# Kernel optimization log

Measured on AMD Instinct MI355X. Metric: run time of the kernel, lower is better.

The kernel has to match this reference:

```python
import jax, jax.numpy as jnp
import numpy as np

E = 2048   # embed_dim
H = 16     # num query heads
D = E // H # head_dim = 128
B = 2
S = 2048


def setup_inputs() -> dict:
    key = jax.random.key(0)
    ks = jax.random.split(key, 12)
    sc = 0.02
    return {
        "input": jax.random.normal(ks[0], (B, S, E), jnp.float32),
        "kv": jax.random.normal(ks[1], (B, S, E), jnp.float32),
        "Wq": jax.random.normal(ks[2], (E, E), jnp.float32) * sc,
        "bq": jnp.zeros((E,), jnp.float32),
        "Wk": jax.random.normal(ks[3], (D, E), jnp.float32) * sc,
        "bk": jnp.zeros((D,), jnp.float32),
        "Wv": jax.random.normal(ks[4], (D, E), jnp.float32) * sc,
        "bv": jnp.zeros((D,), jnp.float32),
        "Wo": jax.random.normal(ks[5], (E, E), jnp.float32) * sc,
        "bo": jnp.zeros((E,), jnp.float32),
        "expanding_context": 0,
    }


def reference(input, kv, Wq, bq, Wk, bk, Wv, bv, Wo, bo, expanding_context):
    b, s, _ = input.shape
    # projections (torch Linear: x @ W.T + b)
    q = (input @ Wq.T + bq).reshape(b, s, H, D).transpose(0, 2, 1, 3)  # [B,H,S,D]
    k = kv @ Wk.T + bk  # [B,S,D] single KV head
    v = kv @ Wv.T + bv  # [B,S,D]
    # scores with single KV head broadcast across query heads
    scores = jnp.einsum('bhsd,btd->bhst', q, k) / jnp.sqrt(jnp.float32(D))
    causal = jnp.triu(jnp.ones((s, s), bool), k=1)  # True above diagonal
    scores = jnp.where(causal[None, None], jnp.float32(-jnp.inf), scores)
    attn = jax.nn.softmax(scores, axis=-1)
    out = jnp.einsum('bhst,btd->bhsd', attn, v)  # [B,H,S,D]
    out = out.transpose(0, 2, 1, 3).reshape(b, s, E)
    return out @ Wo.T + bo
```

## Files before the change

### kernel.cpp

```cpp
#include <hip/hip_runtime.h>

#define B_  2
#define S_  2048
#define E_  2048
#define H_  16
#define D_  128
#define BS_ (B_*S_)

typedef __bf16 bf16_t;
typedef __bf16 bf16x8 __attribute__((ext_vector_type(8)));
typedef __bf16 bf16x4 __attribute__((ext_vector_type(4)));
typedef float  f32x4  __attribute__((ext_vector_type(4)));
typedef float  f32x16 __attribute__((ext_vector_type(16)));

#define QSCALE 0.1275174131003543f

__device__ __forceinline__ void gld16(const bf16_t* g, bf16_t* l) {
    __builtin_amdgcn_global_load_lds(
        (const __attribute__((address_space(1))) void*)g,
        (__attribute__((address_space(3))) void*)l,
        16, 0, 0);
}

__global__ void cvt_all(const float* __restrict__ s0, const float* __restrict__ s1,
                        const float* __restrict__ s2, const float* __restrict__ s3,
                        const float* __restrict__ s4, const float* __restrict__ s5,
                        bf16_t* d0, bf16_t* d1, bf16_t* d2,
                        bf16_t* d3, bf16_t* d4, bf16_t* d5)
{
    long i = ((long)blockIdx.x * blockDim.x + threadIdx.x) * 4;
    const float* s; bf16_t* d;
    if      (i <  8388608) { s = s0; d = d0; }
    else if (i < 16777216) { s = s1; d = d1; i -=  8388608; }
    else if (i < 20971520) { s = s2; d = d2; i -= 16777216; }
    else if (i < 21233664) { s = s3; d = d3; i -= 20971520; }
    else if (i < 21495808) { s = s4; d = d4; i -= 21233664; }
    else                   { s = s5; d = d5; i -= 21495808; }
    float4 v = *(const float4*)(s + i);
    bf16x4 o;
    o[0] = (bf16_t)v.x; o[1] = (bf16_t)v.y; o[2] = (bf16_t)v.z; o[3] = (bf16_t)v.w;
    *(bf16x4*)(d + i) = o;
}

template<int EP>
__device__ __forceinline__ void gemm_tile64(
    const bf16_t* __restrict__ A, const bf16_t* __restrict__ W,
    const float* __restrict__ biasA, const float* __restrict__ biasB,
    float* __restrict__ Cf, bf16_t* __restrict__ Cb,
    int N, int K, float scale, int m0, int w_n0, int c_n0,
    bf16_t* As, bf16_t* Bs)
{
    const int tid  = threadIdx.x;
    const int wave = tid >> 6, lane = tid & 63;
    const int wm = wave >> 1, wn = wave & 1;
    const int lrow = lane & 15, quad = lane >> 4;
    const int r8 = lane >> 3, c8 = (lane & 7) << 3;

    f32x4 acc[4][2] = {};

    for (int k0 = 0; k0 < K; k0 += 64) {
        __syncthreads();
#pragma unroll
        for (int j = 0; j < 4; ++j) {
            int base = (wave * 4 + j) * 8;
            gld16(A + (size_t)(m0 + base + r8) * K + k0 + c8, &As[base * 64]);
        }
#pragma unroll
        for (int j = 0; j < 2; ++j) {
            int base = (wave * 2 + j) * 8;
            gld16(W + (size_t)(w_n0 + base + r8) * K + k0 + c8, &Bs[base * 64]);
        }
        __syncthreads();
#pragma unroll
        for (int ks = 0; ks < 2; ++ks) {
            bf16x8 af[4], bfr[2];
#pragma unroll
            for (int mt = 0; mt < 4; ++mt)
                af[mt] = *(const bf16x8*)&As[(wm * 64 + mt * 16 + lrow) * 64 + ks * 32 + quad * 8];
#pragma unroll
            for (int nt = 0; nt < 2; ++nt)
                bfr[nt] = *(const bf16x8*)&Bs[(wn * 32 + nt * 16 + lrow) * 64 + ks * 32 + quad * 8];
#pragma unroll
            for (int mt = 0; mt < 4; ++mt)
#pragma unroll
                for (int nt = 0; nt < 2; ++nt)
                    acc[mt][nt] = __builtin_amdgcn_mfma_f32_16x16x32_bf16(
                        af[mt], bfr[nt], acc[mt][nt], 0, 0, 0);
        }
    }

#pragma unroll
    for (int mt = 0; mt < 4; ++mt) {
#pragma unroll
        for (int nt = 0; nt < 2; ++nt) {
            int nn = wn * 32 + nt * 16 + lrow;
            int col = c_n0 + nn;
            float bvv = (EP == 1 && biasB && col >= 128) ? biasB[col - 128]
                                                         : biasA[col];
#pragma unroll
            for (int r = 0; r < 4; ++r) {
                int row = m0 + wm * 64 + mt * 16 + quad * 4 + r;
                float v = (acc[mt][nt][r] + bvv) * scale;
                if (EP == 0) Cf[(size_t)row * N + col] = v;
                else         Cb[(size_t)row * N + col] = (bf16_t)v;
            }
        }
    }
}

__global__ __launch_bounds__(256) void gemm_qkv(
    const bf16_t* __restrict__ xb, const bf16_t* __restrict__ kvb,
    const bf16_t* __restrict__ Wq, const bf16_t* __restrict__ Wkv,
    const float* __restrict__ bq, const float* __restrict__ bk,
    const float* __restrict__ bv,
    bf16_t* __restrict__ Qb, bf16_t* __restrict__ KVb)
{
    __shared__ __align__(16) bf16_t As[128 * 64];
    __shared__ __align__(16) bf16_t Bs[64 * 64];
    const int m0 = blockIdx.y * 128;
    if (blockIdx.x < 32) {
        int n0 = blockIdx.x * 64;
        gemm_tile64<1>(xb, Wq, bq, nullptr, nullptr, Qb, E_, E_, QSCALE,
                       m0, n0, n0, As, Bs);
    } else {
        int n0 = (blockIdx.x - 32) * 64;
        gemm_tile64<1>(kvb, Wkv, bk, bv, nullptr, KVb, 256, E_, 1.0f,
                       m0, n0, n0, As, Bs);
    }
}

__global__ __launch_bounds__(256) void gemm_o(
    const bf16_t* __restrict__ A, const bf16_t* __restrict__ W,
    const float* __restrict__ bias, float* __restrict__ Cf)
{
    __shared__ __align__(16) bf16_t As[128 * 64];
    __shared__ __align__(16) bf16_t Bs[64 * 64];
    int n0 = blockIdx.x * 64;
    gemm_tile64<0>(A, W, bias, nullptr, Cf, nullptr, E_, E_, 1.0f,
                   blockIdx.y * 128, n0, n0, As, Bs);
}

__global__ __launch_bounds__(256, 2) void mqa_attn(
    const bf16_t* __restrict__ Q, const bf16_t* __restrict__ KV,
    bf16_t* __restrict__ O)
{
    __shared__ __align__(16) bf16_t Kt[2][64][136];
    __shared__ __align__(16) bf16_t Vt[2][128][72];
    __shared__ float rsl[4][32];

    const int bx = blockIdx.x, h = blockIdx.y, b = blockIdx.z;
    const int qb = b ? bx : (15 - bx);
    const int tid = threadIdx.x, wave = tid >> 6, lane = tid & 63;
    const int ln = lane & 31, hi = lane >> 5;
    const int q0w = qb * 128 + wave * 32;

    const bf16_t* kvp = KV + (size_t)(b * S_) * 256;

    bf16x8 qf[8];
    {
        const bf16_t* qp = Q + ((size_t)(b * S_ + q0w + ln)) * E_ + h * D_ + hi * 8;
#pragma unroll
        for (int st = 0; st < 8; ++st) qf[st] = *(const bf16x8*)(qp + st * 16);
    }

    f32x16 oacc[4] = {};
    bf16x8 af[4] = {};
    float rs0 = 0.f, rs1 = 0.f, rs2 = 0.f, rs3 = 0.f;

    const int NT = 2 * qb + 2;
    const int Tw = (q0w + 31) >> 6;

    bf16x8 kreg[4], vreg[4];
    auto loadKV = [&](int kt) {
        const int k0 = kt * 64;
#pragma unroll
        for (int i = 0; i < 4; ++i) {
            int c = tid + 256 * i;
            kreg[i] = *(const bf16x8*)(kvp + (size_t)(k0 + (c >> 4)) * 256 + ((c & 15) << 3));
            int n = c & 63, d0 = (c >> 6) << 3;
            vreg[i] = *(const bf16x8*)(kvp + (size_t)(k0 + n) * 256 + 128 + d0);
        }
    };
    auto stageWrite = [&](int bb) {
#pragma unroll
        for (int i = 0; i < 4; ++i) {
            int c = tid + 256 * i;
            *(bf16x8*)&Kt[bb][c >> 4][(c & 15) << 3] = kreg[i];
            int n = c & 63, d0 = (c >> 6) << 3;
#pragma unroll
            for (int j = 0; j < 8; ++j) Vt[bb][d0 + j][n] = vreg[i][j];
        }
    };
    auto doPV = [&](int vb) {
        __builtin_amdgcn_s_setprio(1);
#pragma unroll
        for (int ks = 0; ks < 4; ++ks)
#pragma unroll
            for (int dt = 0; dt < 4; ++dt) {
                bf16x8 vf = *(const bf16x8*)&Vt[vb][dt * 32 + ln][ks * 16 + hi * 8];
                oacc[dt] = __builtin_amdgcn_mfma_f32_32x32x16_bf16(af[ks], vf, oacc[dt], 0, 0, 0);
            }
        __builtin_amdgcn_s_setprio(0);
    };

    loadKV(0);
    stageWrite(0);
    if (NT > 1) loadKV(1);

    for (int t = 0; t < NT; ++t) {
        const int cur = t & 1;
        if (t >= 1 && t - 1 <= Tw) doPV(cur ^ 1);
        __syncthreads();
        if (t + 1 < NT) stageWrite(cur ^ 1);
        if (t + 2 < NT) loadKV(t + 2);
        if (t <= Tw) {
            f32x16 sc[2] = {f32x16{}, f32x16{}};
            __builtin_amdgcn_s_setprio(1);
#pragma unroll
            for (int st = 0; st < 8; ++st) {
                bf16x8 qv = qf[st];
#pragma unroll
                for (int ct = 0; ct < 2; ++ct) {
                    bf16x8 kf = *(const bf16x8*)&Kt[cur][ct * 32 + ln][st * 16 + hi * 8];
                    sc[ct] = __builtin_amdgcn_mfma_f32_32x32x16_bf16(kf, qv, sc[ct], 0, 0, 0);
                }
            }
            __builtin_amdgcn_s_setprio(0);
            const int k_base = t * 64;
            const int qi = q0w + ln;
            if (k_base + 63 > q0w) {
#pragma unroll
                for (int ct = 0; ct < 2; ++ct)
#pragma unroll
                    for (int r = 0; r < 16; ++r) {
                        int kj = k_base + ct * 32 + (r & 3) + 8 * (r >> 2) + 4 * hi;
                        float s = (kj > qi) ? -1e30f : sc[ct][r];
                        float pv = exp2f(fminf(s, 110.f));
                        if ((r & 3) == 0) rs0 += pv;
                        else if ((r & 3) == 1) rs1 += pv;
                        else if ((r & 3) == 2) rs2 += pv;
                        else rs3 += pv;
                        sc[ct][r] = pv;
                    }
            } else {
#pragma unroll
                for (int ct = 0; ct < 2; ++ct)
#pragma unroll
                    for (int r = 0; r < 16; ++r) {
                        float pv = exp2f(fminf(sc[ct][r], 110.f));
                        if ((r & 3) == 0) rs0 += pv;
                        else if ((r & 3) == 1) rs1 += pv;
                        else if ((r & 3) == 2) rs2 += pv;
                        else rs3 += pv;
                        sc[ct][r] = pv;
                    }
            }
#pragma unroll
            for (int ks = 0; ks < 4; ++ks) {
                const int c = ks >> 1, b8 = (ks & 1) * 8;
                union { bf16_t h[2]; unsigned u; } pk0, pk1, pk2, pk3;
                pk0.h[0] = (bf16_t)sc[c][b8 + 0]; pk0.h[1] = (bf16_t)sc[c][b8 + 1];
                pk1.h[0] = (bf16_t)sc[c][b8 + 2]; pk1.h[1] = (bf16_t)sc[c][b8 + 3];
                pk2.h[0] = (bf16_t)sc[c][b8 + 4]; pk2.h[1] = (bf16_t)sc[c][b8 + 5];
                pk3.h[0] = (bf16_t)sc[c][b8 + 6]; pk3.h[1] = (bf16_t)sc[c][b8 + 7];
                const unsigned U0 = pk0.u, U1 = pk1.u, U2 = pk2.u, U3 = pk3.u;
                const unsigned V0 = __shfl_xor(U0, 32);
                const unsigned V1 = __shfl_xor(U1, 32);
                const unsigned V2 = __shfl_xor(U2, 32);
                const unsigned V3 = __shfl_xor(U3, 32);
                union { unsigned u[4]; bf16x8 v; } W;
                W.u[0] = hi ? V2 : U0;
                W.u[1] = hi ? V3 : U1;
                W.u[2] = hi ? U2 : V0;
                W.u[3] = hi ? U3 : V1;
                af[ks] = W.v;
            }
        }
    }
    if (Tw == NT - 1) doPV(1);

    float rs = (rs0 + rs1) + (rs2 + rs3);
    rs += __shfl_xor(rs, 32);
    __syncthreads();
    if (lane < 32) rsl[wave][ln] = 1.0f / rs;
    __syncthreads();
#pragma unroll
    for (int dt = 0; dt < 4; ++dt)
#pragma unroll
        for (int r = 0; r < 16; ++r) {
            int ro = (r & 3) + 8 * (r >> 2) + 4 * hi;
            O[((size_t)(b * S_ + q0w + ro)) * E_ + h * D_ + dt * 32 + ln] =
                (bf16_t)(oacc[dt][r] * rsl[wave][ro]);
        }
}

extern "C" void kernel_launch(void* const* d_in, const int* in_sizes, int n_in,
                              void* d_out, int out_size, void* d_ws, size_t ws_size,
                              hipStream_t stream)
{
    const float* x   = (const float*)d_in[0];
    const float* kv  = (const float*)d_in[1];
    const float* Wq  = (const float*)d_in[2];
    const float* bq  = (const float*)d_in[3];
    const float* Wk  = (const float*)d_in[4];
    const float* bk  = (const float*)d_in[5];
    const float* Wv  = (const float*)d_in[6];
    const float* bv  = (const float*)d_in[7];
    const float* Wo  = (const float*)d_in[8];
    const float* bo  = (const float*)d_in[9];
    float* out = (float*)d_out;

    bf16_t* p    = (bf16_t*)d_ws;
    bf16_t* xb   = p;  p += (size_t)BS_ * E_;
    bf16_t* kvb  = p;  p += (size_t)BS_ * E_;
    bf16_t* Wqb  = p;  p += (size_t)E_ * E_;
    bf16_t* Wkvb = p;  p += (size_t)2 * D_ * E_;
    bf16_t* Wob  = p;  p += (size_t)E_ * E_;
    bf16_t* Qb   = p;  p += (size_t)BS_ * E_;
    bf16_t* KVb  = p;  p += (size_t)BS_ * 256;
    bf16_t* Ob   = p;  p += (size_t)BS_ * E_;

    cvt_all<<<dim3(25088), dim3(256), 0, stream>>>(
        x, kv, Wq, Wk, Wv, Wo,
        xb, kvb, Wqb, Wkvb, Wkvb + (size_t)D_ * E_, Wob);

    gemm_qkv<<<dim3(36, BS_ / 128), 256, 0, stream>>>(
        xb, kvb, Wqb, Wkvb, bq, bk, bv, Qb, KVb);

    mqa_attn<<<dim3(S_ / 128, H_, B_), 256, 0, stream>>>(Qb, KVb, Ob);

    gemm_o<<<dim3(E_ / 64, BS_ / 128), 256, 0, stream>>>(Ob, Wob, bo, out);
}
```

Before: 356.6 us.

## Use 128x128 GEMM tiles, MFMA row sums, and paired V transpose stores

The QKV and output-projection GEMMs move from 128x64 to 128x128 tiles, which doubles per-wave MFMA work per A-fragment load and halves the grid. In attention, the softmax row sums come from an MFMA against a ones vector instead of scalar accumulation, which removes the final LDS reduction and its barriers. V staging now packs two adjacent keys into 32-bit LDS writes. Risks: the exp2 clamp at 110 is removed, the row sum is taken from bf16-rounded probabilities, the larger accumulators raise register pressure, and the halved GEMM grids reduce occupancy.

```diff
diff --git a/kernel.cpp b/kernel.cpp
--- a/kernel.cpp
+++ b/kernel.cpp
@@ -43,9 +43,9 @@
 }
 
 template<int EP>
-__device__ __forceinline__ void gemm_tile64(
+__device__ __forceinline__ void gemm_tile128(
     const bf16_t* __restrict__ A, const bf16_t* __restrict__ W,
-    const float* __restrict__ biasA, const float* __restrict__ biasB,
+    const float* __restrict__ bias,
     float* __restrict__ Cf, bf16_t* __restrict__ Cb,
     int N, int K, float scale, int m0, int w_n0, int c_n0,
     bf16_t* As, bf16_t* Bs)
@@ -56,7 +56,7 @@
     const int lrow = lane & 15, quad = lane >> 4;
     const int r8 = lane >> 3, c8 = (lane & 7) << 3;
 
-    f32x4 acc[4][2] = {};
+    f32x4 acc[4][4] = {};
 
     for (int k0 = 0; k0 < K; k0 += 64) {
         __syncthreads();
@@ -66,24 +66,24 @@
             gld16(A + (size_t)(m0 + base + r8) * K + k0 + c8, &As[base * 64]);
         }
 #pragma unroll
-        for (int j = 0; j < 2; ++j) {
-            int base = (wave * 2 + j) * 8;
+        for (int j = 0; j < 4; ++j) {
+            int base = (wave * 4 + j) * 8;
             gld16(W + (size_t)(w_n0 + base + r8) * K + k0 + c8, &Bs[base * 64]);
         }
         __syncthreads();
 #pragma unroll
         for (int ks = 0; ks < 2; ++ks) {
-            bf16x8 af[4], bfr[2];
+            bf16x8 af[4], bfr[4];
 #pragma unroll
             for (int mt = 0; mt < 4; ++mt)
                 af[mt] = *(const bf16x8*)&As[(wm * 64 + mt * 16 + lrow) * 64 + ks * 32 + quad * 8];
 #pragma unroll
-            for (int nt = 0; nt < 2; ++nt)
-                bfr[nt] = *(const bf16x8*)&Bs[(wn * 32 + nt * 16 + lrow) * 64 + ks * 32 + quad * 8];
+            for (int nt = 0; nt < 4; ++nt)
+                bfr[nt] = *(const bf16x8*)&Bs[(wn * 64 + nt * 16 + lrow) * 64 + ks * 32 + quad * 8];
 #pragma unroll
             for (int mt = 0; mt < 4; ++mt)
 #pragma unroll
-                for (int nt = 0; nt < 2; ++nt)
+                for (int nt = 0; nt < 4; ++nt)
                     acc[mt][nt] = __builtin_amdgcn_mfma_f32_16x16x32_bf16(
                         af[mt], bfr[nt], acc[mt][nt], 0, 0, 0);
         }
@@ -92,11 +92,10 @@
 #pragma unroll
     for (int mt = 0; mt < 4; ++mt) {
 #pragma unroll
-        for (int nt = 0; nt < 2; ++nt) {
-            int nn = wn * 32 + nt * 16 + lrow;
-            int col = c_n0 + nn;
-            float bvv = (EP == 1 && biasB && col >= 128) ? biasB[col - 128]
-                                                         : biasA[col];
+        for (int nt = 0; nt < 4; ++nt) {
+            int lcol = wn * 64 + nt * 16 + lrow;
+            int col = c_n0 + lcol;
+            float bvv = bias[lcol];
 #pragma unroll
             for (int r = 0; r < 4; ++r) {
                 int row = m0 + wm * 64 + mt * 16 + quad * 4 + r;
@@ -116,16 +115,19 @@
     bf16_t* __restrict__ Qb, bf16_t* __restrict__ KVb)
 {
     __shared__ __align__(16) bf16_t As[128 * 64];
-    __shared__ __align__(16) bf16_t Bs[64 * 64];
+    __shared__ __align__(16) bf16_t Bs[128 * 64];
     const int m0 = blockIdx.y * 128;
-    if (blockIdx.x < 32) {
-        int n0 = blockIdx.x * 64;
-        gemm_tile64<1>(xb, Wq, bq, nullptr, nullptr, Qb, E_, E_, QSCALE,
-                       m0, n0, n0, As, Bs);
+    const int x = blockIdx.x;
+    if (x < 16) {
+        int n0 = x * 128;
+        gemm_tile128<1>(xb, Wq, bq + n0, nullptr, Qb, E_, E_, QSCALE,
+                        m0, n0, n0, As, Bs);
+    } else if (x == 16) {
+        gemm_tile128<1>(kvb, Wkv, bk, nullptr, KVb, 256, E_, 1.0f,
+                        m0, 0, 0, As, Bs);
     } else {
-        int n0 = (blockIdx.x - 32) * 64;
-        gemm_tile64<1>(kvb, Wkv, bk, bv, nullptr, KVb, 256, E_, 1.0f,
-                       m0, n0, n0, As, Bs);
+        gemm_tile128<1>(kvb, Wkv, bv, nullptr, KVb, 256, E_, 1.0f,
+                        m0, 128, 128, As, Bs);
     }
 }
 
@@ -134,10 +136,10 @@
     const float* __restrict__ bias, float* __restrict__ Cf)
 {
     __shared__ __align__(16) bf16_t As[128 * 64];
-    __shared__ __align__(16) bf16_t Bs[64 * 64];
-    int n0 = blockIdx.x * 64;
-    gemm_tile64<0>(A, W, bias, nullptr, Cf, nullptr, E_, E_, 1.0f,
-                   blockIdx.y * 128, n0, n0, As, Bs);
+    __shared__ __align__(16) bf16_t Bs[128 * 64];
+    int n0 = blockIdx.x * 128;
+    gemm_tile128<0>(A, W, bias + n0, Cf, nullptr, E_, E_, 1.0f,
+                    blockIdx.y * 128, n0, n0, As, Bs);
 }
 
 __global__ __launch_bounds__(256, 2) void mqa_attn(
@@ -146,7 +148,6 @@
 {
     __shared__ __align__(16) bf16_t Kt[2][64][136];
     __shared__ __align__(16) bf16_t Vt[2][128][72];
-    __shared__ float rsl[4][32];
 
     const int bx = blockIdx.x, h = blockIdx.y, b = blockIdx.z;
     const int qb = b ? bx : (15 - bx);
@@ -163,22 +164,32 @@
         for (int st = 0; st < 8; ++st) qf[st] = *(const bf16x8*)(qp + st * 16);
     }
 
+    bf16x8 ones;
+#pragma unroll
+    for (int j = 0; j < 8; ++j) ones[j] = (bf16_t)1.0f;
+
     f32x16 oacc[4] = {};
+    f32x16 racc = {};
     bf16x8 af[4] = {};
-    float rs0 = 0.f, rs1 = 0.f, rs2 = 0.f, rs3 = 0.f;
 
     const int NT = 2 * qb + 2;
     const int Tw = (q0w + 31) >> 6;
 
-    bf16x8 kreg[4], vreg[4];
+    bf16x8 kreg[4], vA[2], vB[2];
     auto loadKV = [&](int kt) {
         const int k0 = kt * 64;
 #pragma unroll
         for (int i = 0; i < 4; ++i) {
             int c = tid + 256 * i;
             kreg[i] = *(const bf16x8*)(kvp + (size_t)(k0 + (c >> 4)) * 256 + ((c & 15) << 3));
-            int n = c & 63, d0 = (c >> 6) << 3;
-            vreg[i] = *(const bf16x8*)(kvp + (size_t)(k0 + n) * 256 + 128 + d0);
+        }
+#pragma unroll
+        for (int i = 0; i < 2; ++i) {
+            int c = tid + 256 * i;
+            int n = (c & 31) * 2, d0 = (c >> 5) << 3;
+            const bf16_t* src = kvp + (size_t)(k0 + n) * 256 + 128 + d0;
+            vA[i] = *(const bf16x8*)src;
+            vB[i] = *(const bf16x8*)(src + 256);
         }
     };
     auto stageWrite = [&](int bb) {
@@ -186,9 +197,17 @@
         for (int i = 0; i < 4; ++i) {
             int c = tid + 256 * i;
             *(bf16x8*)&Kt[bb][c >> 4][(c & 15) << 3] = kreg[i];
-            int n = c & 63, d0 = (c >> 6) << 3;
-#pragma unroll
-            for (int j = 0; j < 8; ++j) Vt[bb][d0 + j][n] = vreg[i][j];
+        }
+#pragma unroll
+        for (int i = 0; i < 2; ++i) {
+            int c = tid + 256 * i;
+            int n = (c & 31) * 2, d0 = (c >> 5) << 3;
+#pragma unroll
+            for (int j = 0; j < 8; ++j) {
+                union { bf16_t h[2]; unsigned u; } w2;
+                w2.h[0] = vA[i][j]; w2.h[1] = vB[i][j];
+                *(unsigned*)&Vt[bb][d0 + j][n] = w2.u;
+            }
         }
     };
     auto doPV = [&](int vb) {
@@ -235,25 +254,14 @@
                     for (int r = 0; r < 16; ++r) {
                         int kj = k_base + ct * 32 + (r & 3) + 8 * (r >> 2) + 4 * hi;
                         float s = (kj > qi) ? -1e30f : sc[ct][r];
-                        float pv = exp2f(fminf(s, 110.f));
-                        if ((r & 3) == 0) rs0 += pv;
-                        else if ((r & 3) == 1) rs1 += pv;
-                        else if ((r & 3) == 2) rs2 += pv;
-                        else rs3 += pv;
-                        sc[ct][r] = pv;
+                        sc[ct][r] = exp2f(s);
                     }
             } else {
 #pragma unroll
                 for (int ct = 0; ct < 2; ++ct)
 #pragma unroll
-                    for (int r = 0; r < 16; ++r) {
-                        float pv = exp2f(fminf(sc[ct][r], 110.f));
-                        if ((r & 3) == 0) rs0 += pv;
-                        else if ((r & 3) == 1) rs1 += pv;
-                        else if ((r & 3) == 2) rs2 += pv;
-                        else rs3 += pv;
-                        sc[ct][r] = pv;
-                    }
+                    for (int r = 0; r < 16; ++r)
+                        sc[ct][r] = exp2f(sc[ct][r]);
             }
 #pragma unroll
             for (int ks = 0; ks < 4; ++ks) {
@@ -275,22 +283,23 @@
                 W.u[3] = hi ? U3 : V1;
                 af[ks] = W.v;
             }
+#pragma unroll
+            for (int ks = 0; ks < 4; ++ks)
+                racc = __builtin_amdgcn_mfma_f32_32x32x16_bf16(af[ks], ones, racc, 0, 0, 0);
         }
     }
     if (Tw == NT - 1) doPV(1);
 
-    float rs = (rs0 + rs1) + (rs2 + rs3);
-    rs += __shfl_xor(rs, 32);
-    __syncthreads();
-    if (lane < 32) rsl[wave][ln] = 1.0f / rs;
-    __syncthreads();
+    float inv[16];
+#pragma unroll
+    for (int r = 0; r < 16; ++r) inv[r] = 1.0f / racc[r];
 #pragma unroll
     for (int dt = 0; dt < 4; ++dt)
 #pragma unroll
         for (int r = 0; r < 16; ++r) {
             int ro = (r & 3) + 8 * (r >> 2) + 4 * hi;
             O[((size_t)(b * S_ + q0w + ro)) * E_ + h * D_ + dt * 32 + ln] =
-                (bf16_t)(oacc[dt][r] * rsl[wave][ro]);
+                (bf16_t)(oacc[dt][r] * inv[r]);
         }
 }
 
@@ -324,10 +333,10 @@
         x, kv, Wq, Wk, Wv, Wo,
         xb, kvb, Wqb, Wkvb, Wkvb + (size_t)D_ * E_, Wob);
 
-    gemm_qkv<<<dim3(36, BS_ / 128), 256, 0, stream>>>(
+    gemm_qkv<<<dim3(18, BS_ / 128), 256, 0, stream>>>(
         xb, kvb, Wqb, Wkvb, bq, bk, bv, Qb, KVb);
 
     mqa_attn<<<dim3(S_ / 128, H_, B_), 256, 0, stream>>>(Qb, KVb, Ob);
 
-    gemm_o<<<dim3(E_ / 64, BS_ / 128), 256, 0, stream>>>(Ob, Wob, bo, out);
-}
+    gemm_o<<<dim3(E_ / 128, BS_ / 128), 256, 0, stream>>>(Ob, Wob, bo, out);
+}
```

Result: no change. 357.4 us (+0.2%).
